# Kernel optimization log

Hardware: AMD Instinct MI355X
Metric: run time of the kernel (lower is better)

The kernel has to match this reference:

```python
import jax, jax.numpy as jnp
import numpy as np

TOP_K = 2  # routing_method: renormalize top-2 (topk then softmax over selected logits)


def setup_inputs() -> dict:
    key = jax.random.key(0)
    ks = jax.random.split(key, 5)
    T, H, I, E = 4096, 1024, 4096, 8
    return {
        "hidden_states": jax.random.normal(ks[0], (T, H), jnp.float32),
        "router_logits": jax.random.normal(ks[1], (T, E), jnp.float32),
        "W_gate": jax.random.normal(ks[2], (E, H, I), jnp.float32) * 0.02,  # w1
        "W_up": jax.random.normal(ks[3], (E, H, I), jnp.float32) * 0.02,   # w3
        "W_down": jax.random.normal(ks[4], (E, I, H), jnp.float32) * 0.02, # w2
    }


def reference(hidden_states, router_logits, W_gate, W_up, W_down):
    # Routing: top-k logits, renormalize with softmax over selected logits.
    top_vals, top_idx = jax.lax.top_k(router_logits, TOP_K)        # [T, K]
    routing_weights = jax.nn.softmax(top_vals, axis=-1)            # [T, K]

    E = W_gate.shape[0]
    out = jnp.zeros_like(hidden_states)                            # [T, H]
    for e in range(E):  # fixed small expert loop (structurally distinct weights)
        # combine weight for expert e per token (0 if not routed here)
        w_e = jnp.sum(jnp.where(top_idx == e, routing_weights, 0.0), axis=-1)  # [T]
        gate = hidden_states @ W_gate[e]                           # [T, I]
        up = hidden_states @ W_up[e]                               # [T, I]
        y = (jax.nn.silu(gate) * up) @ W_down[e]                   # [T, H]
        out = out + w_e[:, None] * y
    return out
```

## Files before the change

### kernel.cpp

```cpp
#include <hip/hip_runtime.h>

typedef float    f32x4 __attribute__((ext_vector_type(4)));
typedef _Float16 f16x8 __attribute__((ext_vector_type(8)));
typedef _Float16 f16x4 __attribute__((ext_vector_type(4)));

#define T_TOK 4096
#define HD    1024
#define ID    4096
#define NE    8
#define TOTP  (2*T_TOK)
#define MAXT1 72
#define MAXT2 40

#define WS_CNT   0
#define WS_FILL  64
#define WS_OFF   128
#define WS_TOT   192
#define WS_TOT2  196
#define WS_TEXP  256
#define WS_TM0   (256 + 4*MAXT1)
#define WS_TEXP2 (256 + 8*MAXT1)
#define WS_TM02  (256 + 8*MAXT1 + 4*MAXT2)
#define WS_TOPE  2048
#define WS_TOPW  (WS_TOPE + 4*TOTP)
#define WS_PAIR  (WS_TOPW + 4*TOTP)
#define WS_ACT   ((size_t)1 << 20)
constexpr size_t WS_YBUF = WS_ACT  + 2ull*TOTP*ID;
constexpr size_t WS_HS16 = WS_YBUF + 2ull*TOTP*HD;
constexpr size_t WS_WG16 = WS_HS16 + 2ull*T_TOK*HD;
constexpr size_t WS_WU16 = WS_WG16 + 2ull*NE*HD*ID;
constexpr size_t WS_WD16 = WS_WU16 + 2ull*NE*HD*ID;

__device__ __forceinline__ void gll16(const void* g, void* l) {
  __builtin_amdgcn_global_load_lds(
      (const __attribute__((address_space(1))) unsigned int*)g,
      (__attribute__((address_space(3))) unsigned int*)l, 16, 0, 0);
}

#define WAITV(N) do { \
    asm volatile("s_waitcnt vmcnt(" #N ")" ::: "memory"); \
    __builtin_amdgcn_sched_barrier(0); \
  } while (0)

__device__ __forceinline__ int lofs(int row, int g) {
  return row * 32 + ((g ^ ((row >> 1) & 3)) << 3);
}

__global__ void k_router(const float* __restrict__ logits, char* __restrict__ ws) {
  int t = blockIdx.x * blockDim.x + threadIdx.x;
  if (t >= T_TOK) return;
  float v0 = -1e30f, v1 = -1e30f; int i0 = 0, i1 = 0;
  #pragma unroll
  for (int e = 0; e < NE; ++e) {
    float v = logits[t * NE + e];
    if (v > v0)      { v1 = v0; i1 = i0; v0 = v; i0 = e; }
    else if (v > v1) { v1 = v;  i1 = e; }
  }
  float w0 = 1.f / (1.f + __expf(v1 - v0));
  ((int*)(ws + WS_TOPE))[2*t]   = i0;
  ((int*)(ws + WS_TOPE))[2*t+1] = i1;
  ((float*)(ws + WS_TOPW))[2*t]   = w0;
  ((float*)(ws + WS_TOPW))[2*t+1] = 1.f - w0;
  atomicAdd(&((int*)(ws + WS_CNT))[i0], 1);
  atomicAdd(&((int*)(ws + WS_CNT))[i1], 1);
}

__global__ void k_prefix(char* __restrict__ ws) {
  if (threadIdx.x != 0 || blockIdx.x != 0) return;
  const int* cnt = (const int*)(ws + WS_CNT);
  int* off   = (int*)(ws + WS_OFF);
  int* texp  = (int*)(ws + WS_TEXP);
  int* tm0   = (int*)(ws + WS_TM0);
  int* texp2 = (int*)(ws + WS_TEXP2);
  int* tm02  = (int*)(ws + WS_TM02);
  int run = 0, t1 = 0, t2 = 0;
  for (int e = 0; e < NE; ++e) {
    off[e] = run;
    int ne = cnt[e];
    for (int i = 0; i < ne; i += 128) { texp[t1] = e; tm0[t1] = i; ++t1; }
    for (int i = 0; i < ne; i += 256) { texp2[t2] = e; tm02[t2] = i; ++t2; }
    run += ne;
  }
  off[NE] = run;
  *(int*)(ws + WS_TOT)  = t1;
  *(int*)(ws + WS_TOT2) = t2;
}

__global__ void k_scatter(char* __restrict__ ws) {
  int t = blockIdx.x * blockDim.x + threadIdx.x;
  if (t >= T_TOK) return;
  const int* tope = (const int*)(ws + WS_TOPE);
  const int* off  = (const int*)(ws + WS_OFF);
  int* fill = (int*)(ws + WS_FILL);
  int* pair = (int*)(ws + WS_PAIR);
  #pragma unroll
  for (int s = 0; s < 2; ++s) {
    int id = 2*t + s;
    int e = tope[id];
    int pos = off[e] + atomicAdd(&fill[e], 1);
    pair[pos] = id;
  }
}

__global__ void k_hscvt(const float* __restrict__ src, _Float16* __restrict__ dst) {
  int i = blockIdx.x * blockDim.x + threadIdx.x;
  f32x4 v = ((const f32x4*)src)[i];
  f16x4 o;
  #pragma unroll
  for (int j = 0; j < 4; ++j) o[j] = (_Float16)v[j];
  ((f16x4*)dst)[i] = o;
}

__global__ __launch_bounds__(256) void k_wtrans(const float* __restrict__ src,
                                                _Float16* __restrict__ dst,
                                                int K, int N) {
  const int e = blockIdx.z;
  const int n0 = blockIdx.x * 64, k0 = blockIdx.y * 64;
  const float* s = src + (size_t)e * K * N;
  _Float16* d = dst + (size_t)e * (size_t)K * N;
  __shared__ _Float16 t[64][68];
  const int tx = threadIdx.x & 15, ty = threadIdx.x >> 4;
  #pragma unroll
  for (int it = 0; it < 4; ++it) {
    int k = k0 + it*16 + ty;
    f32x4 v = *(const f32x4*)&s[(size_t)k * N + n0 + tx*4];
    #pragma unroll
    for (int j = 0; j < 4; ++j) t[tx*4 + j][it*16 + ty] = (_Float16)v[j];
  }
  __syncthreads();
  #pragma unroll
  for (int it = 0; it < 4; ++it) {
    int n = it*16 + ty;
    *(f16x4*)&d[(size_t)(n0 + n) * K + k0 + tx*4] = *(const f16x4*)&t[n][tx*4];
  }
}

#define G1_BUF 12288
__global__ __launch_bounds__(256, 2) void k_gemm1(
    const _Float16* __restrict__ hs16, const _Float16* __restrict__ WgT,
    const _Float16* __restrict__ WuT, char* __restrict__ ws) {
  const int s = blockIdx.y;
  if (s >= *(const int*)(ws + WS_TOT)) return;
  const int e    = ((const int*)(ws + WS_TEXP))[s];
  const int m0   = ((const int*)(ws + WS_TM0))[s];
  const int offE = ((const int*)(ws + WS_OFF))[e];
  const int nE   = ((const int*)(ws + WS_CNT))[e];
  _Float16* __restrict__ act = (_Float16*)(ws + WS_ACT);
  const int n0 = blockIdx.x * 128;
  const int tid = threadIdx.x, lane = tid & 63, wid = tid >> 6;

  __shared__ __align__(16) _Float16 sm[3 * G1_BUF];

  const int rL = lane >> 2;
  const int q  = (((lane & 3) ^ ((lane >> 3) & 3)) << 3);
  const _Float16 *aS[2], *gS[2], *uS[2];
  #pragma unroll
  for (int j = 0; j < 2; ++j) {
    int mm = m0 + 32*wid + 16*j + rL;
    int tok = (mm < nE) ? (((const int*)(ws + WS_PAIR))[offE + mm] >> 1) : 0;
    aS[j] = hs16 + (size_t)tok * HD + q;
    size_t cB = (size_t)e * ID + (n0 + 32*wid + 16*j + rL);
    gS[j] = WgT + cB * HD + q;
    uS[j] = WuT + cB * HD + q;
  }

  auto stage = [&](int buf, int kt) {
    _Float16* b = sm + buf * G1_BUF + wid*1024;
    const int ko = kt * 32;
    #pragma unroll
    for (int j = 0; j < 2; ++j) {
      gll16(aS[j] + ko, b + j*512);
      gll16(gS[j] + ko, b + 4096 + j*512);
      gll16(uS[j] + ko, b + 8192 + j*512);
    }
  };

  const int wr = wid >> 1, wc = wid & 1;
  const int l15 = lane & 15, l4 = lane >> 4;
  f32x4 accg[4][4] = {}, accu[4][4] = {};

  auto compute = [&](int buf) {
    const _Float16* b0 = sm + buf * G1_BUF;
    f16x8 afr[4], bfr[4];
    #pragma unroll
    for (int i = 0; i < 4; ++i)
      afr[i] = *(const f16x8*)&b0[lofs(64*wr + 16*i + l15, l4)];
    #pragma unroll
    for (int j = 0; j < 4; ++j)
      bfr[j] = *(const f16x8*)&b0[4096 + lofs(64*wc + 16*j + l15, l4)];
    __builtin_amdgcn_s_setprio(1);
    #pragma unroll
    for (int i = 0; i < 4; ++i)
      #pragma unroll
      for (int j = 0; j < 4; ++j)
        accg[i][j] = __builtin_amdgcn_mfma_f32_16x16x32_f16(afr[i], bfr[j], accg[i][j], 0, 0, 0);
    __builtin_amdgcn_s_setprio(0);
    #pragma unroll
    for (int j = 0; j < 4; ++j)
      bfr[j] = *(const f16x8*)&b0[8192 + lofs(64*wc + 16*j + l15, l4)];
    __builtin_amdgcn_s_setprio(1);
    #pragma unroll
    for (int i = 0; i < 4; ++i)
      #pragma unroll
      for (int j = 0; j < 4; ++j)
        accu[i][j] = __builtin_amdgcn_mfma_f32_16x16x32_f16(afr[i], bfr[j], accu[i][j], 0, 0, 0);
    __builtin_amdgcn_s_setprio(0);
  };

  auto step = [&](int t, int cur, int nb) {
    stage(nb, t + 2);
    WAITV(12);
    __builtin_amdgcn_s_barrier();
    compute(cur);
    __builtin_amdgcn_s_barrier();
  };

  const int KT = HD / 32;
  stage(0, 0); stage(1, 1);
  for (int t = 0; t < KT - 2; t += 3) {
    step(t,     0, 2);
    step(t + 1, 1, 0);
    step(t + 2, 2, 1);
  }
  WAITV(6);
  __builtin_amdgcn_s_barrier();
  compute(0);
  __builtin_amdgcn_s_barrier();
  WAITV(0);
  __builtin_amdgcn_s_barrier();
  compute(1);

  #pragma unroll
  for (int i = 0; i < 4; ++i)
    #pragma unroll
    for (int r = 0; r < 4; ++r) {
      const int mm = m0 + 64*wr + 16*i + 4*l4 + r;
      if (mm < nE) {
        const size_t prow = (size_t)(offE + mm) * ID;
        #pragma unroll
        for (int j = 0; j < 4; ++j) {
          float g = accg[i][j][r], u = accu[i][j][r];
          float sv = g / (1.f + __expf(-g)) * u;
          act[prow + n0 + 64*wc + 16*j + l15] = (_Float16)sv;
        }
      }
    }
}

#define G2_BUF 12288
__global__ __launch_bounds__(256, 2) void k_gemm2(const _Float16* __restrict__ WdT,
                                                  char* __restrict__ ws) {
  const int s = blockIdx.y;
  if (s >= *(const int*)(ws + WS_TOT2)) return;
  const int e    = ((const int*)(ws + WS_TEXP2))[s];
  const int m0   = ((const int*)(ws + WS_TM02))[s];
  const int offE = ((const int*)(ws + WS_OFF))[e];
  const int nE   = ((const int*)(ws + WS_CNT))[e];
  const int* __restrict__ pair = (const int*)(ws + WS_PAIR);
  const _Float16* __restrict__ act = (const _Float16*)(ws + WS_ACT);
  _Float16* __restrict__ ybuf = (_Float16*)(ws + WS_YBUF);
  const int n0 = blockIdx.x * 128;
  const int tid = threadIdx.x, lane = tid & 63, wid = tid >> 6;

  __shared__ __align__(16) _Float16 sm[3 * G2_BUF];

  const int rL = lane >> 2;
  const int q  = (((lane & 3) ^ ((lane >> 3) & 3)) << 3);
  const _Float16 *aS[4], *bS[2];
  #pragma unroll
  for (int j = 0; j < 4; ++j) {
    int mm = m0 + 64*wid + 16*j + rL;
    int p = (mm < nE) ? (offE + mm) : offE;
    aS[j] = act + (size_t)p * ID + q;
  }
  #pragma unroll
  for (int j = 0; j < 2; ++j)
    bS[j] = WdT + ((size_t)e * HD + (n0 + 32*wid + 16*j + rL)) * ID + q;

  auto stage = [&](int buf, int kt) {
    _Float16* b = sm + buf * G2_BUF;
    const int ko = kt * 32;
    #pragma unroll
    for (int j = 0; j < 4; ++j) gll16(aS[j] + ko, b + wid*2048 + j*512);
    #pragma unroll
    for (int j = 0; j < 2; ++j) gll16(bS[j] + ko, b + 8192 + wid*1024 + j*512);
  };

  const int wr = wid >> 1, wc = wid & 1;
  const int l15 = lane & 15, l4 = lane >> 4;
  f32x4 acc[8][4] = {};

  auto compute = [&](int buf) {
    const _Float16* b0 = sm + buf * G2_BUF;
    f16x8 afr[8], bfr[4];
    #pragma unroll
    for (int i = 0; i < 8; ++i)
      afr[i] = *(const f16x8*)&b0[lofs(128*wr + 16*i + l15, l4)];
    #pragma unroll
    for (int j = 0; j < 4; ++j)
      bfr[j] = *(const f16x8*)&b0[8192 + lofs(64*wc + 16*j + l15, l4)];
    __builtin_amdgcn_s_setprio(1);
    #pragma unroll
    for (int i = 0; i < 8; ++i)
      #pragma unroll
      for (int j = 0; j < 4; ++j)
        acc[i][j] = __builtin_amdgcn_mfma_f32_16x16x32_f16(afr[i], bfr[j], acc[i][j], 0, 0, 0);
    __builtin_amdgcn_s_setprio(0);
  };

  auto step = [&](int t, int cur, int nb) {
    stage(nb, t + 2);
    WAITV(12);
    __builtin_amdgcn_s_barrier();
    compute(cur);
    __builtin_amdgcn_s_barrier();
  };

  const int KT = ID / 32;
  stage(0, 0); stage(1, 1);
  for (int t = 0; t < KT - 2; t += 3) {
    step(t,     0, 2);
    step(t + 1, 1, 0);
    step(t + 2, 2, 1);
  }
  WAITV(6);
  __builtin_amdgcn_s_barrier();
  compute(0);
  __builtin_amdgcn_s_barrier();
  WAITV(0);
  __builtin_amdgcn_s_barrier();
  compute(1);

  #pragma unroll
  for (int i = 0; i < 8; ++i)
    #pragma unroll
    for (int r = 0; r < 4; ++r) {
      const int mm = m0 + 128*wr + 16*i + 4*l4 + r;
      if (mm < nE) {
        const int id = pair[offE + mm];
        #pragma unroll
        for (int j = 0; j < 4; ++j)
          ybuf[(size_t)id * HD + n0 + 64*wc + 16*j + l15] = (_Float16)acc[i][j][r];
      }
    }
}

__global__ void k_combine(const char* __restrict__ ws, float* __restrict__ out) {
  const int idx = blockIdx.x * blockDim.x + threadIdx.x;
  const int t = idx >> 7, c = idx & 127;
  const float* topw = (const float*)(ws + WS_TOPW);
  const _Float16* yb = (const _Float16*)(ws + WS_YBUF);
  f16x8 y0 = ((const f16x8*)(yb + (size_t)(2*t)     * HD))[c];
  f16x8 y1 = ((const f16x8*)(yb + (size_t)(2*t + 1) * HD))[c];
  const float w0 = topw[2*t], w1 = topw[2*t+1];
  f32x4 o0, o1;
  #pragma unroll
  for (int j = 0; j < 4; ++j) {
    o0[j] = w0 * (float)y0[j]     + w1 * (float)y1[j];
    o1[j] = w0 * (float)y0[4 + j] + w1 * (float)y1[4 + j];
  }
  ((f32x4*)out)[2*idx]     = o0;
  ((f32x4*)out)[2*idx + 1] = o1;
}

extern "C" void kernel_launch(void* const* d_in, const int* in_sizes, int n_in,
                              void* d_out, int out_size, void* d_ws, size_t ws_size,
                              hipStream_t stream) {
  const float* hs     = (const float*)d_in[0];
  const float* logits = (const float*)d_in[1];
  const float* Wg     = (const float*)d_in[2];
  const float* Wu     = (const float*)d_in[3];
  const float* Wd     = (const float*)d_in[4];
  char* ws = (char*)d_ws;

  _Float16* hs16 = (_Float16*)(ws + WS_HS16);
  _Float16* wg16 = (_Float16*)(ws + WS_WG16);
  _Float16* wu16 = (_Float16*)(ws + WS_WU16);
  _Float16* wd16 = (_Float16*)(ws + WS_WD16);

  hipMemsetAsync(ws, 0, 256, stream);
  k_router <<<dim3(T_TOK/256), dim3(256), 0, stream>>>(logits, ws);
  k_prefix <<<dim3(1),         dim3(64),  0, stream>>>(ws);
  k_scatter<<<dim3(T_TOK/256), dim3(256), 0, stream>>>(ws);
  k_hscvt  <<<dim3(T_TOK*HD/4/256), dim3(256), 0, stream>>>(hs, hs16);
  k_wtrans <<<dim3(ID/64, HD/64, NE), dim3(256), 0, stream>>>(Wg, wg16, HD, ID);
  k_wtrans <<<dim3(ID/64, HD/64, NE), dim3(256), 0, stream>>>(Wu, wu16, HD, ID);
  k_wtrans <<<dim3(HD/64, ID/64, NE), dim3(256), 0, stream>>>(Wd, wd16, ID, HD);
  k_gemm1  <<<dim3(ID/128, MAXT1), dim3(256), 0, stream>>>(hs16, wg16, wu16, ws);
  k_gemm2  <<<dim3(HD/128, MAXT2), dim3(256), 0, stream>>>(wd16, ws);
  k_combine<<<dim3(T_TOK*HD/8/256), dim3(256), 0, stream>>>(ws, (float*)d_out);
}
```

Baseline: 506.7 us.

## Enlarge gemm1 tile to 256 rows with 512 threads and K=64 double buffering

```diff
diff --git a/kernel.cpp b/kernel.cpp
--- a/kernel.cpp
+++ b/kernel.cpp
@@ -45,6 +45,9 @@
 __device__ __forceinline__ int lofs(int row, int g) {
   return row * 32 + ((g ^ ((row >> 1) & 3)) << 3);
 }
+__device__ __forceinline__ int lofs64(int row, int g8) {
+  return row * 64 + ((g8 ^ (row & 7)) << 3);
+}
 
 __global__ void k_router(const float* __restrict__ logits, char* __restrict__ ws) {
   int t = blockIdx.x * blockDim.x + threadIdx.x;
@@ -135,113 +138,105 @@
   }
 }
 
-#define G1_BUF 12288
-__global__ __launch_bounds__(256, 2) void k_gemm1(
+__global__ __launch_bounds__(512, 2) void k_gemm1(
     const _Float16* __restrict__ hs16, const _Float16* __restrict__ WgT,
     const _Float16* __restrict__ WuT, char* __restrict__ ws) {
   const int s = blockIdx.y;
-  if (s >= *(const int*)(ws + WS_TOT)) return;
-  const int e    = ((const int*)(ws + WS_TEXP))[s];
-  const int m0   = ((const int*)(ws + WS_TM0))[s];
+  if (s >= *(const int*)(ws + WS_TOT2)) return;
+  const int e    = ((const int*)(ws + WS_TEXP2))[s];
+  const int m0   = ((const int*)(ws + WS_TM02))[s];
   const int offE = ((const int*)(ws + WS_OFF))[e];
   const int nE   = ((const int*)(ws + WS_CNT))[e];
   _Float16* __restrict__ act = (_Float16*)(ws + WS_ACT);
   const int n0 = blockIdx.x * 128;
   const int tid = threadIdx.x, lane = tid & 63, wid = tid >> 6;
 
-  __shared__ __align__(16) _Float16 sm[3 * G1_BUF];
-
-  const int rL = lane >> 2;
-  const int q  = (((lane & 3) ^ ((lane >> 3) & 3)) << 3);
-  const _Float16 *aS[2], *gS[2], *uS[2];
-  #pragma unroll
-  for (int j = 0; j < 2; ++j) {
-    int mm = m0 + 32*wid + 16*j + rL;
-    int tok = (mm < nE) ? (((const int*)(ws + WS_PAIR))[offE + mm] >> 1) : 0;
-    aS[j] = hs16 + (size_t)tok * HD + q;
-    size_t cB = (size_t)e * ID + (n0 + 32*wid + 16*j + rL);
-    gS[j] = WgT + cB * HD + q;
-    uS[j] = WuT + cB * HD + q;
-  }
-
-  auto stage = [&](int buf, int kt) {
-    _Float16* b = sm + buf * G1_BUF + wid*1024;
-    const int ko = kt * 32;
+  __shared__ __align__(16) _Float16 sm[2 * 32768];
+
+  const int r8 = lane >> 3;
+  const int q64 = (((lane & 7) ^ r8) << 3);
+  const int* __restrict__ pairp = (const int*)(ws + WS_PAIR);
+  const _Float16 *aP[4], *gP[2], *uP[2];
+  #pragma unroll
+  for (int c = 0; c < 4; ++c) {
+    int mm = m0 + 32*wid + 8*c + r8;
+    int tok = (mm < nE) ? (pairp[offE + mm] >> 1) : 0;
+    aP[c] = hs16 + (size_t)tok * HD + q64;
+  }
+  #pragma unroll
+  for (int c = 0; c < 2; ++c) {
+    size_t col = (size_t)e * ID + (n0 + 16*wid + 8*c + r8);
+    gP[c] = WgT + col * HD + q64;
+    uP[c] = WuT + col * HD + q64;
+  }
+
+  auto stage8 = [&](int buf, int kt) {
+    _Float16* base = sm + buf * 32768;
+    const int ko = kt * 64;
+    #pragma unroll
+    for (int c = 0; c < 4; ++c)
+      gll16(aP[c] + ko, base + (32*wid + 8*c) * 64);
+    #pragma unroll
+    for (int c = 0; c < 2; ++c) {
+      gll16(gP[c] + ko, base + 16384 + (16*wid + 8*c) * 64);
+      gll16(uP[c] + ko, base + 24576 + (16*wid + 8*c) * 64);
+    }
+  };
+
+  const int wr = wid >> 2, wc = wid & 3;
+  const int l15 = lane & 15, l4 = lane >> 4;
+  f32x4 accg[8][2] = {}, accu[8][2] = {};
+
+  auto computeKK = [&](int buf, int kk) {
+    const _Float16* b0 = sm + buf * 32768;
+    f16x8 afr[8], bg[2], bu[2];
+    #pragma unroll
+    for (int i = 0; i < 8; ++i) {
+      const int row = 128*wr + 16*i + l15;
+      afr[i] = *(const f16x8*)&b0[lofs64(row, kk*4 + l4)];
+    }
     #pragma unroll
     for (int j = 0; j < 2; ++j) {
-      gll16(aS[j] + ko, b + j*512);
-      gll16(gS[j] + ko, b + 4096 + j*512);
-      gll16(uS[j] + ko, b + 8192 + j*512);
-    }
-  };
-
-  const int wr = wid >> 1, wc = wid & 1;
-  const int l15 = lane & 15, l4 = lane >> 4;
-  f32x4 accg[4][4] = {}, accu[4][4] = {};
-
-  auto compute = [&](int buf) {
-    const _Float16* b0 = sm + buf * G1_BUF;
-    f16x8 afr[4], bfr[4];
-    #pragma unroll
-    for (int i = 0; i < 4; ++i)
-      afr[i] = *(const f16x8*)&b0[lofs(64*wr + 16*i + l15, l4)];
-    #pragma unroll
-    for (int j = 0; j < 4; ++j)
-      bfr[j] = *(const f16x8*)&b0[4096 + lofs(64*wc + 16*j + l15, l4)];
+      const int row = 32*wc + 16*j + l15;
+      bg[j] = *(const f16x8*)&b0[16384 + lofs64(row, kk*4 + l4)];
+      bu[j] = *(const f16x8*)&b0[24576 + lofs64(row, kk*4 + l4)];
+    }
     __builtin_amdgcn_s_setprio(1);
     #pragma unroll
-    for (int i = 0; i < 4; ++i)
+    for (int i = 0; i < 8; ++i)
       #pragma unroll
-      for (int j = 0; j < 4; ++j)
-        accg[i][j] = __builtin_amdgcn_mfma_f32_16x16x32_f16(afr[i], bfr[j], accg[i][j], 0, 0, 0);
+      for (int j = 0; j < 2; ++j) {
+        accg[i][j] = __builtin_amdgcn_mfma_f32_16x16x32_f16(afr[i], bg[j], accg[i][j], 0, 0, 0);
+        accu[i][j] = __builtin_amdgcn_mfma_f32_16x16x32_f16(afr[i], bu[j], accu[i][j], 0, 0, 0);
+      }
     __builtin_amdgcn_s_setprio(0);
-    #pragma unroll
-    for (int j = 0; j < 4; ++j)
-      bfr[j] = *(const f16x8*)&b0[8192 + lofs(64*wc + 16*j + l15, l4)];
-    __builtin_amdgcn_s_setprio(1);
-    #pragma unroll
-    for (int i = 0; i < 4; ++i)
-      #pragma unroll
-      for (int j = 0; j < 4; ++j)
-        accu[i][j] = __builtin_amdgcn_mfma_f32_16x16x32_f16(afr[i], bfr[j], accu[i][j], 0, 0, 0);
-    __builtin_amdgcn_s_setprio(0);
-  };
-
-  auto step = [&](int t, int cur, int nb) {
-    stage(nb, t + 2);
-    WAITV(12);
-    __builtin_amdgcn_s_barrier();
-    compute(cur);
-    __builtin_amdgcn_s_barrier();
-  };
-
-  const int KT = HD / 32;
-  stage(0, 0); stage(1, 1);
-  for (int t = 0; t < KT - 2; t += 3) {
-    step(t,     0, 2);
-    step(t + 1, 1, 0);
-    step(t + 2, 2, 1);
-  }
-  WAITV(6);
-  __builtin_amdgcn_s_barrier();
-  compute(0);
-  __builtin_amdgcn_s_barrier();
+  };
+
+  const int KT = HD / 64;
+  stage8(0, 0);
   WAITV(0);
   __builtin_amdgcn_s_barrier();
-  compute(1);
-
-  #pragma unroll
-  for (int i = 0; i < 4; ++i)
+  for (int t = 0; t < KT; ++t) {
+    const int cur = t & 1;
+    if (t + 1 < KT) stage8(cur ^ 1, t + 1);
+    computeKK(cur, 0);
+    computeKK(cur, 1);
+    WAITV(0);
+    __builtin_amdgcn_s_barrier();
+  }
+
+  #pragma unroll
+  for (int i = 0; i < 8; ++i)
     #pragma unroll
     for (int r = 0; r < 4; ++r) {
-      const int mm = m0 + 64*wr + 16*i + 4*l4 + r;
+      const int mm = m0 + 128*wr + 16*i + 4*l4 + r;
       if (mm < nE) {
         const size_t prow = (size_t)(offE + mm) * ID;
         #pragma unroll
-        for (int j = 0; j < 4; ++j) {
+        for (int j = 0; j < 2; ++j) {
           float g = accg[i][j][r], u = accu[i][j][r];
           float sv = g / (1.f + __expf(-g)) * u;
-          act[prow + n0 + 64*wc + 16*j + l15] = (_Float16)sv;
+          act[prow + n0 + 32*wc + 16*j + l15] = (_Float16)sv;
         }
       }
     }
@@ -386,7 +381,7 @@
   k_wtrans <<<dim3(ID/64, HD/64, NE), dim3(256), 0, stream>>>(Wg, wg16, HD, ID);
   k_wtrans <<<dim3(ID/64, HD/64, NE), dim3(256), 0, stream>>>(Wu, wu16, HD, ID);
   k_wtrans <<<dim3(HD/64, ID/64, NE), dim3(256), 0, stream>>>(Wd, wd16, ID, HD);
-  k_gemm1  <<<dim3(ID/128, MAXT1), dim3(256), 0, stream>>>(hs16, wg16, wu16, ws);
+  k_gemm1  <<<dim3(ID/128, MAXT2), dim3(512), 0, stream>>>(hs16, wg16, wu16, ws);
   k_gemm2  <<<dim3(HD/128, MAXT2), dim3(256), 0, stream>>>(wd16, ws);
   k_combine<<<dim3(T_TOK*HD/8/256), dim3(256), 0, stream>>>(ws, (float*)d_out);
 }
```

Result: no change. 501.1 us (-1.1%).

## Retile both expert GEMMs and split down-projection K into two partial buffers

Applied to the files above, without the earlier changes.

```diff
diff --git a/kernel.cpp b/kernel.cpp
--- a/kernel.cpp
+++ b/kernel.cpp
@@ -30,6 +30,8 @@
 constexpr size_t WS_WG16 = WS_HS16 + 2ull*T_TOK*HD;
 constexpr size_t WS_WU16 = WS_WG16 + 2ull*NE*HD*ID;
 constexpr size_t WS_WD16 = WS_WU16 + 2ull*NE*HD*ID;
+constexpr size_t WS_YB0  = WS_WG16;
+constexpr size_t WS_YB1  = WS_WG16 + 2ull*TOTP*HD;
 
 __device__ __forceinline__ void gll16(const void* g, void* l) {
   __builtin_amdgcn_global_load_lds(
@@ -135,100 +137,190 @@
   }
 }
 
-#define G1_BUF 12288
-__global__ __launch_bounds__(256, 2) void k_gemm1(
+#define G1_BUF 16384
+__global__ __launch_bounds__(512, 2) void k_gemm1(
     const _Float16* __restrict__ hs16, const _Float16* __restrict__ WgT,
     const _Float16* __restrict__ WuT, char* __restrict__ ws) {
+  const int s = blockIdx.y;
+  if (s >= *(const int*)(ws + WS_TOT2)) return;
+  const int e    = ((const int*)(ws + WS_TEXP2))[s];
+  const int m0   = ((const int*)(ws + WS_TM02))[s];
+  const int offE = ((const int*)(ws + WS_OFF))[e];
+  const int nE   = ((const int*)(ws + WS_CNT))[e];
+  _Float16* __restrict__ act = (_Float16*)(ws + WS_ACT);
+  const int n0 = blockIdx.x * 128;
+  const int tid = threadIdx.x, lane = tid & 63, wid = tid >> 6;
+
+  __shared__ __align__(16) _Float16 sm[4 * G1_BUF];
+
+  const int rL = lane >> 2;
+  const int q  = (((lane & 3) ^ ((lane >> 3) & 3)) << 3);
+  const int* __restrict__ pairp = (const int*)(ws + WS_PAIR);
+  const _Float16 *aP[2], *gP, *uP;
+  #pragma unroll
+  for (int c = 0; c < 2; ++c) {
+    int mm = m0 + 32*wid + 16*c + rL;
+    int tok = (mm < nE) ? (pairp[offE + mm] >> 1) : 0;
+    aP[c] = hs16 + (size_t)tok * HD + q;
+  }
+  {
+    size_t col = (size_t)e * ID + (n0 + 16*wid + rL);
+    gP = WgT + col * HD + q;
+    uP = WuT + col * HD + q;
+  }
+
+  auto stage = [&](int buf, int kt) {
+    _Float16* b = sm + buf * G1_BUF;
+    const int ko = kt * 32;
+    gll16(aP[0] + ko, b + (32*wid) * 32);
+    gll16(aP[1] + ko, b + (32*wid + 16) * 32);
+    gll16(gP + ko, b + 8192  + (16*wid) * 32);
+    gll16(uP + ko, b + 12288 + (16*wid) * 32);
+  };
+
+  const int wr = wid >> 2, wc = wid & 3;
+  const int l15 = lane & 15, l4 = lane >> 4;
+  f32x4 accg[8][2] = {}, accu[8][2] = {};
+
+  auto compute = [&](int buf) {
+    const _Float16* b0 = sm + buf * G1_BUF;
+    f16x8 afr[8], bg[2], bu[2];
+    #pragma unroll
+    for (int i = 0; i < 8; ++i)
+      afr[i] = *(const f16x8*)&b0[lofs(128*wr + 16*i + l15, l4)];
+    #pragma unroll
+    for (int j = 0; j < 2; ++j) {
+      bg[j] = *(const f16x8*)&b0[8192  + lofs(32*wc + 16*j + l15, l4)];
+      bu[j] = *(const f16x8*)&b0[12288 + lofs(32*wc + 16*j + l15, l4)];
+    }
+    __builtin_amdgcn_s_setprio(1);
+    #pragma unroll
+    for (int i = 0; i < 8; ++i)
+      #pragma unroll
+      for (int j = 0; j < 2; ++j) {
+        accg[i][j] = __builtin_amdgcn_mfma_f32_16x16x32_f16(afr[i], bg[j], accg[i][j], 0, 0, 0);
+        accu[i][j] = __builtin_amdgcn_mfma_f32_16x16x32_f16(afr[i], bu[j], accu[i][j], 0, 0, 0);
+      }
+    __builtin_amdgcn_s_setprio(0);
+  };
+
+  const int KT = HD / 32;
+  stage(0, 0); stage(1, 1); stage(2, 2);
+  for (int t = 0; t < KT - 3; ++t) {
+    stage((t + 3) & 3, t + 3);
+    WAITV(12);
+    __builtin_amdgcn_s_barrier();
+    compute(t & 3);
+    __builtin_amdgcn_s_barrier();
+  }
+  WAITV(8);
+  __builtin_amdgcn_s_barrier();
+  compute((KT - 3) & 3);
+  __builtin_amdgcn_s_barrier();
+  WAITV(4);
+  __builtin_amdgcn_s_barrier();
+  compute((KT - 2) & 3);
+  __builtin_amdgcn_s_barrier();
+  WAITV(0);
+  __builtin_amdgcn_s_barrier();
+  compute((KT - 1) & 3);
+
+  #pragma unroll
+  for (int i = 0; i < 8; ++i)
+    #pragma unroll
+    for (int r = 0; r < 4; ++r) {
+      const int mm = m0 + 128*wr + 16*i + 4*l4 + r;
+      if (mm < nE) {
+        const size_t prow = (size_t)(offE + mm) * ID;
+        #pragma unroll
+        for (int j = 0; j < 2; ++j) {
+          float g = accg[i][j][r], u = accu[i][j][r];
+          float sv = g / (1.f + __expf(-g)) * u;
+          act[prow + n0 + 32*wc + 16*j + l15] = (_Float16)sv;
+        }
+      }
+    }
+}
+
+#define G2_BUF 12288
+__global__ __launch_bounds__(256, 2) void k_gemm2(const _Float16* __restrict__ WdT,
+                                                  char* __restrict__ ws) {
   const int s = blockIdx.y;
   if (s >= *(const int*)(ws + WS_TOT)) return;
   const int e    = ((const int*)(ws + WS_TEXP))[s];
   const int m0   = ((const int*)(ws + WS_TM0))[s];
   const int offE = ((const int*)(ws + WS_OFF))[e];
   const int nE   = ((const int*)(ws + WS_CNT))[e];
-  _Float16* __restrict__ act = (_Float16*)(ws + WS_ACT);
-  const int n0 = blockIdx.x * 128;
+  const int h    = blockIdx.z;
+  const int kbase = h * (ID / 2);
+  const int* __restrict__ pair = (const int*)(ws + WS_PAIR);
+  const _Float16* __restrict__ act = (const _Float16*)(ws + WS_ACT);
+  _Float16* __restrict__ yb = (_Float16*)(ws + (h ? WS_YB1 : WS_YB0));
+  const int n0 = blockIdx.x * 256;
   const int tid = threadIdx.x, lane = tid & 63, wid = tid >> 6;
 
-  __shared__ __align__(16) _Float16 sm[3 * G1_BUF];
+  __shared__ __align__(16) _Float16 sm[3 * G2_BUF];
 
   const int rL = lane >> 2;
   const int q  = (((lane & 3) ^ ((lane >> 3) & 3)) << 3);
-  const _Float16 *aS[2], *gS[2], *uS[2];
-  #pragma unroll
-  for (int j = 0; j < 2; ++j) {
-    int mm = m0 + 32*wid + 16*j + rL;
-    int tok = (mm < nE) ? (((const int*)(ws + WS_PAIR))[offE + mm] >> 1) : 0;
-    aS[j] = hs16 + (size_t)tok * HD + q;
-    size_t cB = (size_t)e * ID + (n0 + 32*wid + 16*j + rL);
-    gS[j] = WgT + cB * HD + q;
-    uS[j] = WuT + cB * HD + q;
-  }
+  const _Float16 *aS[2], *bS[4];
+  #pragma unroll
+  for (int c = 0; c < 2; ++c) {
+    int mm = m0 + 32*wid + 16*c + rL;
+    int p = (mm < nE) ? (offE + mm) : offE;
+    aS[c] = act + (size_t)p * ID + kbase + q;
+  }
+  #pragma unroll
+  for (int c = 0; c < 4; ++c)
+    bS[c] = WdT + ((size_t)e * HD + (n0 + 64*wid + 16*c + rL)) * ID + kbase + q;
 
   auto stage = [&](int buf, int kt) {
-    _Float16* b = sm + buf * G1_BUF + wid*1024;
+    _Float16* b = sm + buf * G2_BUF;
     const int ko = kt * 32;
     #pragma unroll
-    for (int j = 0; j < 2; ++j) {
-      gll16(aS[j] + ko, b + j*512);
-      gll16(gS[j] + ko, b + 4096 + j*512);
-      gll16(uS[j] + ko, b + 8192 + j*512);
-    }
+    for (int c = 0; c < 2; ++c) gll16(aS[c] + ko, b + (32*wid + 16*c) * 32);
+    #pragma unroll
+    for (int c = 0; c < 4; ++c) gll16(bS[c] + ko, b + 4096 + (64*wid + 16*c) * 32);
   };
 
   const int wr = wid >> 1, wc = wid & 1;
   const int l15 = lane & 15, l4 = lane >> 4;
-  f32x4 accg[4][4] = {}, accu[4][4] = {};
+  f32x4 acc[4][8] = {};
 
   auto compute = [&](int buf) {
-    const _Float16* b0 = sm + buf * G1_BUF;
-    f16x8 afr[4], bfr[4];
+    const _Float16* b0 = sm + buf * G2_BUF;
+    f16x8 afr[4], bfr[8];
     #pragma unroll
     for (int i = 0; i < 4; ++i)
       afr[i] = *(const f16x8*)&b0[lofs(64*wr + 16*i + l15, l4)];
     #pragma unroll
-    for (int j = 0; j < 4; ++j)
-      bfr[j] = *(const f16x8*)&b0[4096 + lofs(64*wc + 16*j + l15, l4)];
+    for (int j = 0; j < 8; ++j)
+      bfr[j] = *(const f16x8*)&b0[4096 + lofs(128*wc + 16*j + l15, l4)];
     __builtin_amdgcn_s_setprio(1);
     #pragma unroll
     for (int i = 0; i < 4; ++i)
       #pragma unroll
-      for (int j = 0; j < 4; ++j)
-        accg[i][j] = __builtin_amdgcn_mfma_f32_16x16x32_f16(afr[i], bfr[j], accg[i][j], 0, 0, 0);
-    __builtin_amdgcn_s_setprio(0);
-    #pragma unroll
-    for (int j = 0; j < 4; ++j)
-      bfr[j] = *(const f16x8*)&b0[8192 + lofs(64*wc + 16*j + l15, l4)];
-    __builtin_amdgcn_s_setprio(1);
-    #pragma unroll
-    for (int i = 0; i < 4; ++i)
-      #pragma unroll
-      for (int j = 0; j < 4; ++j)
-        accu[i][j] = __builtin_amdgcn_mfma_f32_16x16x32_f16(afr[i], bfr[j], accu[i][j], 0, 0, 0);
+      for (int j = 0; j < 8; ++j)
+        acc[i][j] = __builtin_amdgcn_mfma_f32_16x16x32_f16(afr[i], bfr[j], acc[i][j], 0, 0, 0);
     __builtin_amdgcn_s_setprio(0);
   };
 
-  auto step = [&](int t, int cur, int nb) {
-    stage(nb, t + 2);
+  const int KT = (ID / 2) / 32;
+  stage(0, 0); stage(1, 1);
+  for (int t = 0; t < KT - 2; ++t) {
+    stage((t + 2) % 3, t + 2);
     WAITV(12);
     __builtin_amdgcn_s_barrier();
-    compute(cur);
+    compute(t % 3);
     __builtin_amdgcn_s_barrier();
-  };
-
-  const int KT = HD / 32;
-  stage(0, 0); stage(1, 1);
-  for (int t = 0; t < KT - 2; t += 3) {
-    step(t,     0, 2);
-    step(t + 1, 1, 0);
-    step(t + 2, 2, 1);
   }
   WAITV(6);
   __builtin_amdgcn_s_barrier();
-  compute(0);
+  compute((KT - 2) % 3);
   __builtin_amdgcn_s_barrier();
   WAITV(0);
   __builtin_amdgcn_s_barrier();
-  compute(1);
+  compute((KT - 1) % 3);
 
   #pragma unroll
   for (int i = 0; i < 4; ++i)
@@ -236,111 +328,10 @@
     for (int r = 0; r < 4; ++r) {
       const int mm = m0 + 64*wr + 16*i + 4*l4 + r;
       if (mm < nE) {
-        const size_t prow = (size_t)(offE + mm) * ID;
-        #pragma unroll
-        for (int j = 0; j < 4; ++j) {
-          float g = accg[i][j][r], u = accu[i][j][r];
-          float sv = g / (1.f + __expf(-g)) * u;
-          act[prow + n0 + 64*wc + 16*j + l15] = (_Float16)sv;
-        }
-      }
-    }
-}
-
-#define G2_BUF 12288
-__global__ __launch_bounds__(256, 2) void k_gemm2(const _Float16* __restrict__ WdT,
-                                                  char* __restrict__ ws) {
-  const int s = blockIdx.y;
-  if (s >= *(const int*)(ws + WS_TOT2)) return;
-  const int e    = ((const int*)(ws + WS_TEXP2))[s];
-  const int m0   = ((const int*)(ws + WS_TM02))[s];
-  const int offE = ((const int*)(ws + WS_OFF))[e];
-  const int nE   = ((const int*)(ws + WS_CNT))[e];
-  const int* __restrict__ pair = (const int*)(ws + WS_PAIR);
-  const _Float16* __restrict__ act = (const _Float16*)(ws + WS_ACT);
-  _Float16* __restrict__ ybuf = (_Float16*)(ws + WS_YBUF);
-  const int n0 = blockIdx.x * 128;
-  const int tid = threadIdx.x, lane = tid & 63, wid = tid >> 6;
-
-  __shared__ __align__(16) _Float16 sm[3 * G2_BUF];
-
-  const int rL = lane >> 2;
-  const int q  = (((lane & 3) ^ ((lane >> 3) & 3)) << 3);
-  const _Float16 *aS[4], *bS[2];
-  #pragma unroll
-  for (int j = 0; j < 4; ++j) {
-    int mm = m0 + 64*wid + 16*j + rL;
-    int p = (mm < nE) ? (offE + mm) : offE;
-    aS[j] = act + (size_t)p * ID + q;
-  }
-  #pragma unroll
-  for (int j = 0; j < 2; ++j)
-    bS[j] = WdT + ((size_t)e * HD + (n0 + 32*wid + 16*j + rL)) * ID + q;
-
-  auto stage = [&](int buf, int kt) {
-    _Float16* b = sm + buf * G2_BUF;
-    const int ko = kt * 32;
-    #pragma unroll
-    for (int j = 0; j < 4; ++j) gll16(aS[j] + ko, b + wid*2048 + j*512);
-    #pragma unroll
-    for (int j = 0; j < 2; ++j) gll16(bS[j] + ko, b + 8192 + wid*1024 + j*512);
-  };
-
-  const int wr = wid >> 1, wc = wid & 1;
-  const int l15 = lane & 15, l4 = lane >> 4;
-  f32x4 acc[8][4] = {};
-
-  auto compute = [&](int buf) {
-    const _Float16* b0 = sm + buf * G2_BUF;
-    f16x8 afr[8], bfr[4];
-    #pragma unroll
-    for (int i = 0; i < 8; ++i)
-      afr[i] = *(const f16x8*)&b0[lofs(128*wr + 16*i + l15, l4)];
-    #pragma unroll
-    for (int j = 0; j < 4; ++j)
-      bfr[j] = *(const f16x8*)&b0[8192 + lofs(64*wc + 16*j + l15, l4)];
-    __builtin_amdgcn_s_setprio(1);
-    #pragma unroll
-    for (int i = 0; i < 8; ++i)
-      #pragma unroll
-      for (int j = 0; j < 4; ++j)
-        acc[i][j] = __builtin_amdgcn_mfma_f32_16x16x32_f16(afr[i], bfr[j], acc[i][j], 0, 0, 0);
-    __builtin_amdgcn_s_setprio(0);
-  };
-
-  auto step = [&](int t, int cur, int nb) {
-    stage(nb, t + 2);
-    WAITV(12);
-    __builtin_amdgcn_s_barrier();
-    compute(cur);
-    __builtin_amdgcn_s_barrier();
-  };
-
-  const int KT = ID / 32;
-  stage(0, 0); stage(1, 1);
-  for (int t = 0; t < KT - 2; t += 3) {
-    step(t,     0, 2);
-    step(t + 1, 1, 0);
-    step(t + 2, 2, 1);
-  }
-  WAITV(6);
-  __builtin_amdgcn_s_barrier();
-  compute(0);
-  __builtin_amdgcn_s_barrier();
-  WAITV(0);
-  __builtin_amdgcn_s_barrier();
-  compute(1);
-
-  #pragma unroll
-  for (int i = 0; i < 8; ++i)
-    #pragma unroll
-    for (int r = 0; r < 4; ++r) {
-      const int mm = m0 + 128*wr + 16*i + 4*l4 + r;
-      if (mm < nE) {
         const int id = pair[offE + mm];
         #pragma unroll
-        for (int j = 0; j < 4; ++j)
-          ybuf[(size_t)id * HD + n0 + 64*wc + 16*j + l15] = (_Float16)acc[i][j][r];
+        for (int j = 0; j < 8; ++j)
+          yb[(size_t)id * HD + n0 + 128*wc + 16*j + l15] = (_Float16)acc[i][j][r];
       }
     }
 }
@@ -349,15 +340,18 @@
   const int idx = blockIdx.x * blockDim.x + threadIdx.x;
   const int t = idx >> 7, c = idx & 127;
   const float* topw = (const float*)(ws + WS_TOPW);
-  const _Float16* yb = (const _Float16*)(ws + WS_YBUF);
-  f16x8 y0 = ((const f16x8*)(yb + (size_t)(2*t)     * HD))[c];
-  f16x8 y1 = ((const f16x8*)(yb + (size_t)(2*t + 1) * HD))[c];
+  const _Float16* y0p = (const _Float16*)(ws + WS_YB0);
+  const _Float16* y1p = (const _Float16*)(ws + WS_YB1);
+  f16x8 a0 = ((const f16x8*)(y0p + (size_t)(2*t)     * HD))[c];
+  f16x8 b0 = ((const f16x8*)(y1p + (size_t)(2*t)     * HD))[c];
+  f16x8 a1 = ((const f16x8*)(y0p + (size_t)(2*t + 1) * HD))[c];
+  f16x8 b1 = ((const f16x8*)(y1p + (size_t)(2*t + 1) * HD))[c];
   const float w0 = topw[2*t], w1 = topw[2*t+1];
   f32x4 o0, o1;
   #pragma unroll
   for (int j = 0; j < 4; ++j) {
-    o0[j] = w0 * (float)y0[j]     + w1 * (float)y1[j];
-    o1[j] = w0 * (float)y0[4 + j] + w1 * (float)y1[4 + j];
+    o0[j] = w0 * ((float)a0[j]     + (float)b0[j])     + w1 * ((float)a1[j]     + (float)b1[j]);
+    o1[j] = w0 * ((float)a0[4 + j] + (float)b0[4 + j]) + w1 * ((float)a1[4 + j] + (float)b1[4 + j]);
   }
   ((f32x4*)out)[2*idx]     = o0;
   ((f32x4*)out)[2*idx + 1] = o1;
@@ -386,7 +380,7 @@
   k_wtrans <<<dim3(ID/64, HD/64, NE), dim3(256), 0, stream>>>(Wg, wg16, HD, ID);
   k_wtrans <<<dim3(ID/64, HD/64, NE), dim3(256), 0, stream>>>(Wu, wu16, HD, ID);
   k_wtrans <<<dim3(HD/64, ID/64, NE), dim3(256), 0, stream>>>(Wd, wd16, ID, HD);
-  k_gemm1  <<<dim3(ID/128, MAXT1), dim3(256), 0, stream>>>(hs16, wg16, wu16, ws);
-  k_gemm2  <<<dim3(HD/128, MAXT2), dim3(256), 0, stream>>>(wd16, ws);
+  k_gemm1  <<<dim3(ID/128, MAXT2),    dim3(512), 0, stream>>>(hs16, wg16, wu16, ws);
+  k_gemm2  <<<dim3(HD/256, MAXT1, 2), dim3(256), 0, stream>>>(wd16, ws);
   k_combine<<<dim3(T_TOK*HD/8/256), dim3(256), 0, stream>>>(ws, (float*)d_out);
 }
```

New measurement: 486.5 us. 1.04x faster.
